# Optimization experiments

Hardware: AMD Instinct MI355X
Metric: run time of the kernel (lower is better)

## Reference

```python
import jax, jax.numpy as jnp
import numpy as np

B, NL, NT = 8, 64, 512   # graphs, ligand atoms/graph, target nodes/graph
CF = 128                 # per-node embedding dim (Linear(256,...) => 2*128)
H = 128                  # hidden_dim
K = 10                   # n_gaussians
E = 1024                 # ligand edges
BN_EPS = 1e-4


def setup_inputs() -> dict:
    key = jax.random.key(0)
    ks = jax.random.split(key, 24)
    inp = {}
    inp["h_l_x"] = jax.random.normal(ks[0], (B * NL, CF), jnp.float32)
    inp["h_t_x"] = jax.random.normal(ks[1], (B * NT, CF), jnp.float32)
    inp["h_l_pos"] = jax.random.normal(ks[2], (B * NL, 3), jnp.float32)
    inp["h_t_pos"] = jax.random.normal(ks[3], (B * NT, 3), jnp.float32)
    inp["edge_index"] = jax.random.randint(ks[4], (2, E), 0, B * NL, jnp.int64)
    s = 0.05
    inp["W1"] = jax.random.normal(ks[5], (2 * CF, H), jnp.float32) * s
    inp["b1"] = jnp.zeros((H,), jnp.float32)
    inp["gamma"] = jnp.ones((H,), jnp.float32)
    inp["beta"] = jnp.zeros((H,), jnp.float32)
    inp["rmean"] = jax.random.normal(ks[6], (H,), jnp.float32) * 0.1
    inp["rvar"] = jax.random.uniform(ks[7], (H,), jnp.float32, 0.5, 1.5)
    inp["Wpi"] = jax.random.normal(ks[8], (H, K), jnp.float32) * s
    inp["bpi"] = jnp.zeros((K,), jnp.float32)
    inp["Wsig"] = jax.random.normal(ks[9], (H, K), jnp.float32) * s
    inp["bsig"] = jnp.zeros((K,), jnp.float32)
    inp["Wmu"] = jax.random.normal(ks[10], (H, K), jnp.float32) * s
    inp["bmu"] = jnp.zeros((K,), jnp.float32)
    inp["Wat"] = jax.random.normal(ks[11], (CF, 28), jnp.float32) * s
    inp["bat"] = jnp.zeros((28,), jnp.float32)
    inp["Wbd"] = jax.random.normal(ks[12], (2 * CF, 6), jnp.float32) * s
    inp["bbd"] = jnp.zeros((6,), jnp.float32)
    return inp


def reference(h_l_x, h_t_x, h_l_pos, h_t_pos, edge_index,
              W1, b1, gamma, beta, rmean, rvar,
              Wpi, bpi, Wsig, bsig, Wmu, bmu, Wat, bat, Wbd, bbd):
    # dense batched node features (equal counts per graph => reshape)
    hl = h_l_x.reshape(B, NL, CF)
    ht = h_t_x.reshape(B, NT, CF)

    # cat([hl_repeat, ht_repeat]) @ W1 == hl@W1[:CF] + ht@W1[CF:] (broadcast add)
    zl = jnp.einsum('blc,ch->blh', hl, W1[:CF])          # [B,NL,H]
    zt = jnp.einsum('btc,ch->bth', ht, W1[CF:])          # [B,NT,H]
    z = zl[:, :, None, :] + zt[:, None, :, :] + b1       # [B,NL,NT,H]
    z = z.reshape(B * NL * NT, H)

    # BatchNorm1d (eval: running stats), ELU; Dropout is identity in eval
    z = (z - rmean) * (gamma / jnp.sqrt(rvar + BN_EPS)) + beta
    C = jax.nn.elu(z)

    pi = jax.nn.softmax(C @ Wpi + bpi, axis=-1)
    sigma = jax.nn.elu(C @ Wsig + bsig) + 1.1
    mu = jax.nn.elu(C @ Wmu + bmu) + 1.0

    # pairwise euclidean distances, detached in original
    pl = h_l_pos.reshape(B, NL, 3)
    pt = h_t_pos.reshape(B, NT, 3)
    d2 = (-2.0 * jnp.einsum('bld,btd->blt', pl, pt)
          + jnp.sum(pt ** 2, -1)[:, None, :]
          + jnp.sum(pl ** 2, -1)[:, :, None])
    dist = jnp.sqrt(d2).reshape(B * NL * NT)
    dist = jax.lax.stop_gradient(dist)[:, None]          # [P,1]

    atom_types = h_l_x @ Wat + bat                       # [B*NL,28]
    eb = jnp.concatenate([h_l_x[edge_index[0]], h_l_x[edge_index[1]]], axis=1)
    bond_types = eb @ Wbd + bbd                          # [E,6]

    C_batch = jnp.repeat(jnp.arange(B, dtype=jnp.int32), NL * NT)
    return (pi, sigma, mu, dist, atom_types, bond_types, C_batch)
```

## Files before the change

kernel.cpp:

```cpp
#include <hip/hip_runtime.h>
#include <hip/hip_bf16.h>
#include <cstdint>
#include <cstddef>

#define NB_B 8
#define NL   64
#define NT   512
#define CF   128
#define HD   128
#define NK   10
#define NE   1024

static constexpr size_t P_TOT    = (size_t)NB_B * NL * NT;
static constexpr size_t PI_OFF   = 0;
static constexpr size_t SIG_OFF  = P_TOT * 10;
static constexpr size_t MU_OFF   = SIG_OFF + P_TOT * 10;
static constexpr size_t DIST_OFF = MU_OFF + P_TOT * 10;
static constexpr size_t AT_OFF   = DIST_OFF + P_TOT;
static constexpr size_t BD_OFF   = AT_OFF + 512 * 28;
static constexpr size_t CB_OFF   = BD_OFF + NE * 6;

typedef __attribute__((ext_vector_type(8))) short short8;
typedef __attribute__((ext_vector_type(4))) float floatx4;
typedef __attribute__((ext_vector_type(2))) float floatx2;

union U8 { short8 s8; unsigned int u[4]; };

__device__ __forceinline__ float bf2f(unsigned short u) {
    return __uint_as_float(((unsigned int)u) << 16);
}
__device__ __forceinline__ unsigned short f2bf(float f) {
    unsigned int x = __float_as_uint(f);
    x = (x + 0x7FFFu + ((x >> 16) & 1u)) >> 16;
    return (unsigned short)x;
}
__device__ __forceinline__ unsigned int pk2bf(float a, float b) {
    __hip_bfloat162 h = __float22bfloat162_rn(make_float2(a, b));
    return *reinterpret_cast<unsigned int*>(&h);
}
__device__ __forceinline__ float elu(float x) {
    return fmaxf(x, 0.f) + (__expf(fminf(x, 0.f)) - 1.f);
}

__global__ __launch_bounds__(256) void k_pre(
    const float* __restrict__ hl,
    const float* __restrict__ ht,
    const int*   __restrict__ eidx,
    const float* __restrict__ W1,
    const float* __restrict__ b1,
    const float* __restrict__ gamma_,
    const float* __restrict__ beta_,
    const float* __restrict__ rmean,
    const float* __restrict__ rvar,
    const float* __restrict__ Wpi,
    const float* __restrict__ Wsig,
    const float* __restrict__ Wmu,
    const float* __restrict__ Wat,
    const float* __restrict__ bat,
    const float* __restrict__ Wbd,
    const float* __restrict__ bbd,
    unsigned short* __restrict__ zl,
    unsigned short* __restrict__ zt,
    unsigned short* __restrict__ wcomb_t,
    float* __restrict__ out_at,
    float* __restrict__ out_bd)
{
    const int blk = blockIdx.x;
    const int tid = threadIdx.x;

    if (blk < 144) {
        const bool is_l = (blk < 16);
        const int rbase = is_l ? blk * 32 : (blk - 16) * 32;
        const float* A  = is_l ? hl : ht;
        const float* Wx = W1 + (is_l ? 0 : (size_t)CF * HD);
        unsigned short* Z = is_l ? zl : zt;

        const int wave = tid >> 6;
        const int lane = tid & 63;
        const int m    = lane & 15;
        const int kq   = (lane >> 4) * 8;
        const int n0   = wave * 32 + m;

        floatx4 acc[2][2];
        #pragma unroll
        for (int i = 0; i < 2; ++i)
            #pragma unroll
            for (int j = 0; j < 2; ++j)
                acc[i][j] = (floatx4){0.f, 0.f, 0.f, 0.f};

        #pragma unroll
        for (int kb = 0; kb < 4; ++kb) {
            const int k0 = kb * 32 + kq;
            short8 a[2];
            #pragma unroll
            for (int mt = 0; mt < 2; ++mt) {
                const float* ap = A + (size_t)(rbase + mt * 16 + m) * CF + k0;
                const float4 f0 = *(const float4*)ap;
                const float4 f1 = *(const float4*)(ap + 4);
                U8 t;
                t.u[0] = pk2bf(f0.x, f0.y);
                t.u[1] = pk2bf(f0.z, f0.w);
                t.u[2] = pk2bf(f1.x, f1.y);
                t.u[3] = pk2bf(f1.z, f1.w);
                a[mt] = t.s8;
            }
            short8 bf[2];
            #pragma unroll
            for (int nt = 0; nt < 2; ++nt) {
                const int n = n0 + nt * 16;
                float w[8];
                #pragma unroll
                for (int j = 0; j < 8; ++j)
                    w[j] = Wx[(size_t)(k0 + j) * HD + n];
                U8 t;
                #pragma unroll
                for (int j = 0; j < 4; ++j) t.u[j] = pk2bf(w[2*j], w[2*j+1]);
                bf[nt] = t.s8;
            }
            #pragma unroll
            for (int mt = 0; mt < 2; ++mt)
                #pragma unroll
                for (int nt = 0; nt < 2; ++nt)
                    acc[mt][nt] = __builtin_amdgcn_mfma_f32_16x16x32_bf16(a[mt], bf[nt], acc[mt][nt], 0, 0, 0);
        }

        #pragma unroll
        for (int nt = 0; nt < 2; ++nt) {
            const int col = n0 + nt * 16;
            const float s   = gamma_[col] * rsqrtf(rvar[col] + 1e-4f);
            const float off = is_l ? 0.f : ((b1[col] - rmean[col]) * s + beta_[col]);
            #pragma unroll
            for (int mt = 0; mt < 2; ++mt)
                #pragma unroll
                for (int r = 0; r < 4; ++r) {
                    const int row = rbase + mt * 16 + (lane >> 4) * 4 + r;
                    Z[(size_t)row * HD + col] = f2bf(acc[mt][nt][r] * s + off);
                }
        }
    } else if (blk == 144) {
        for (int i = tid; i < 32 * HD; i += 256) {
            const int n = i >> 7, k = i & 127;
            float v = 0.f;
            if (n < 10)      v = Wpi [k * NK + n];
            else if (n < 20) v = Wsig[k * NK + (n - 10)];
            else if (n < 30) v = Wmu [k * NK + (n - 20)];
            wcomb_t[i] = f2bf(v);
        }
    } else if (blk < 201) {
        const int oi = (blk - 145) * 256 + tid;
        const int r = oi / 28, n = oi - r * 28;
        float acc = bat[n];
        #pragma unroll 4
        for (int c = 0; c < CF; ++c)
            acc += hl[(size_t)r * CF + c] * Wat[c * 28 + n];
        out_at[oi] = acc;
    } else {
        const int oi = (blk - 201) * 256 + tid;
        const int e = oi / 6, n = oi - e * 6;
        const int s0 = eidx[e], s1 = eidx[NE + e];
        float acc = bbd[n];
        #pragma unroll 4
        for (int c = 0; c < CF; ++c) {
            acc += hl[(size_t)s0 * CF + c] * Wbd[c * 6 + n];
            acc += hl[(size_t)s1 * CF + c] * Wbd[(CF + c) * 6 + n];
        }
        out_bd[oi] = acc;
    }
}

__global__ __launch_bounds__(256) void k_main(
    const unsigned short* __restrict__ zl,
    const unsigned short* __restrict__ zt,
    const unsigned short* __restrict__ wcomb_t,
    const float* __restrict__ bpi,
    const float* __restrict__ bsig,
    const float* __restrict__ bmu,
    const float* __restrict__ hlpos,
    const float* __restrict__ htpos,
    float* __restrict__ out)
{
    __shared__ float Dl[128 * 34];
    __shared__ float biass[32];
    __shared__ float pls[3];

    const int tid  = threadIdx.x;
    const int blk  = blockIdx.x;
    const int b    = blk >> 8;
    const int l    = (blk >> 2) & 63;
    const int ch   = blk & 3;
    const int lane = tid & 63;
    const int wave = tid >> 6;
    const int m    = lane & 15;
    const int quad = lane >> 4;

    if (tid < 32) {
        float v = 0.f;
        if (tid < 10)      v = bpi[tid];
        else if (tid < 20) v = bsig[tid - 10];
        else if (tid < 30) v = bmu[tid - 20];
        biass[tid] = v;
    } else if (tid < 35) {
        pls[tid - 32] = hlpos[(size_t)(b * NL + l) * 3 + (tid - 32)];
    }

    short8 bfrag[2][4];
    #pragma unroll
    for (int nt = 0; nt < 2; ++nt)
        #pragma unroll
        for (int kb = 0; kb < 4; ++kb)
            bfrag[nt][kb] = *(const short8*)(wcomb_t + (size_t)(nt * 16 + m) * HD + kb * 32 + quad * 8);

    const unsigned short* zlr = zl + (size_t)(b * NL + l) * HD;
    const unsigned short* ztb = zt + (size_t)(b * NT + ch * 128) * HD;

    floatx4 acc[2][2];
    #pragma unroll
    for (int i = 0; i < 2; ++i)
        #pragma unroll
        for (int j = 0; j < 2; ++j)
            acc[i][j] = (floatx4){0.f, 0.f, 0.f, 0.f};

    #pragma unroll
    for (int kb = 0; kb < 4; ++kb) {
        const int k0 = kb * 32 + quad * 8;
        const short8 zlv = *(const short8*)(zlr + k0);
        float zf[8];
        #pragma unroll
        for (int j = 0; j < 8; ++j) zf[j] = bf2f((unsigned short)zlv[j]);

        short8 a[2];
        #pragma unroll
        for (int mt = 0; mt < 2; ++mt) {
            const int row = wave * 32 + mt * 16 + m;
            const short8 ztv = *(const short8*)(ztb + (size_t)row * HD + k0);
            float e[8];
            #pragma unroll
            for (int j = 0; j < 8; ++j)
                e[j] = elu(zf[j] + bf2f((unsigned short)ztv[j]));
            U8 t;
            #pragma unroll
            for (int j = 0; j < 4; ++j) t.u[j] = pk2bf(e[2*j], e[2*j+1]);
            a[mt] = t.s8;
        }
        #pragma unroll
        for (int mt = 0; mt < 2; ++mt)
            #pragma unroll
            for (int nt = 0; nt < 2; ++nt)
                acc[mt][nt] = __builtin_amdgcn_mfma_f32_16x16x32_bf16(a[mt], bfrag[nt][kb], acc[mt][nt], 0, 0, 0);
    }

    #pragma unroll
    for (int mt = 0; mt < 2; ++mt)
        #pragma unroll
        for (int nt = 0; nt < 2; ++nt)
            #pragma unroll
            for (int r = 0; r < 4; ++r) {
                const int row = wave * 32 + mt * 16 + quad * 4 + r;
                const int col = nt * 16 + m;
                Dl[row * 34 + col] = acc[mt][nt][r];
            }
    __syncthreads();

    const size_t gp = ((size_t)(b * NL + l)) * NT + ch * 128 + (tid & 127);
    if (tid < 128) {
        const int p = tid;
        float v[10];
        float mx = -1e30f;
        #pragma unroll
        for (int n = 0; n < 10; ++n) {
            v[n] = Dl[p * 34 + n] + biass[n];
            mx = fmaxf(mx, v[n]);
        }
        float s = 0.f;
        #pragma unroll
        for (int n = 0; n < 10; ++n) { v[n] = __expf(v[n] - mx); s += v[n]; }
        const float inv = 1.f / s;
        floatx2* po = (floatx2*)(out + PI_OFF + gp * 10);
        #pragma unroll
        for (int n = 0; n < 5; ++n) po[n] = (floatx2){v[2*n] * inv, v[2*n+1] * inv};
    } else {
        const int p = tid - 128;
        float sg[10], mv[10];
        #pragma unroll
        for (int n = 0; n < 10; ++n) {
            sg[n] = elu(Dl[p * 34 + 10 + n] + biass[10 + n]) + 1.1f;
            mv[n] = elu(Dl[p * 34 + 20 + n] + biass[20 + n]) + 1.0f;
        }
        floatx2* ps = (floatx2*)(out + SIG_OFF + gp * 10);
        floatx2* pm = (floatx2*)(out + MU_OFF  + gp * 10);
        #pragma unroll
        for (int n = 0; n < 5; ++n) {
            ps[n] = (floatx2){sg[2*n], sg[2*n+1]};
            pm[n] = (floatx2){mv[2*n], mv[2*n+1]};
        }
        const int t = ch * 128 + p;
        const size_t pb = (size_t)(b * NT + t) * 3;
        const float dx = pls[0] - htpos[pb + 0];
        const float dy = pls[1] - htpos[pb + 1];
        const float dz = pls[2] - htpos[pb + 2];
        out[DIST_OFF + gp] = sqrtf(dx * dx + dy * dy + dz * dz);
        out[CB_OFF + gp]   = (float)b;
    }
}

extern "C" void kernel_launch(void* const* d_in, const int* in_sizes, int n_in,
                              void* d_out, int out_size, void* d_ws, size_t ws_size,
                              hipStream_t stream)
{
    const float* hl     = (const float*)d_in[0];
    const float* ht     = (const float*)d_in[1];
    const float* hlpos  = (const float*)d_in[2];
    const float* htpos  = (const float*)d_in[3];
    const int*   eidx   = (const int*)d_in[4];
    const float* W1     = (const float*)d_in[5];
    const float* b1     = (const float*)d_in[6];
    const float* gamma_ = (const float*)d_in[7];
    const float* beta_  = (const float*)d_in[8];
    const float* rmean  = (const float*)d_in[9];
    const float* rvar   = (const float*)d_in[10];
    const float* Wpi    = (const float*)d_in[11];
    const float* bpi    = (const float*)d_in[12];
    const float* Wsig   = (const float*)d_in[13];
    const float* bsig   = (const float*)d_in[14];
    const float* Wmu    = (const float*)d_in[15];
    const float* bmu    = (const float*)d_in[16];
    const float* Wat    = (const float*)d_in[17];
    const float* bat    = (const float*)d_in[18];
    const float* Wbd    = (const float*)d_in[19];
    const float* bbd    = (const float*)d_in[20];

    float* out = (float*)d_out;
    unsigned short* ws  = (unsigned short*)d_ws;
    unsigned short* zl      = ws;
    unsigned short* zt      = ws + 512 * 128;
    unsigned short* wcomb_t = ws + 512 * 128 + 4096 * 128;

    k_pre<<<225, 256, 0, stream>>>(hl, ht, eidx, W1, b1, gamma_, beta_, rmean, rvar,
                                   Wpi, Wsig, Wmu, Wat, bat, Wbd, bbd,
                                   zl, zt, wcomb_t, out + AT_OFF, out + BD_OFF);
    k_main<<<2048, 256, 0, stream>>>(zl, zt, wcomb_t, bpi, bsig, bmu, hlpos, htpos, out);
}
```

Measured before the change: 140.4 us.

## Move atom/bond head GEMMs into main kernel using bf16 MFMA

The atom-type and bond-type projections move out of the preprocessing kernel and run as 12 extra blocks at the end of the main kernel's grid. They now use bf16 MFMA tiles instead of scalar fp32 dot-product loops. This shortens the serial pre-kernel, which is on the critical path before k_main, and overlaps the small heads with the main work. The cost is bf16 rounding on these outputs, which may reduce accuracy, plus uncoalesced weight loads.

```diff
diff --git a/kernel.cpp b/kernel.cpp
--- a/kernel.cpp
+++ b/kernel.cpp
@@ -45,7 +45,6 @@
 __global__ __launch_bounds__(256) void k_pre(
     const float* __restrict__ hl,
     const float* __restrict__ ht,
-    const int*   __restrict__ eidx,
     const float* __restrict__ W1,
     const float* __restrict__ b1,
     const float* __restrict__ gamma_,
@@ -55,15 +54,9 @@
     const float* __restrict__ Wpi,
     const float* __restrict__ Wsig,
     const float* __restrict__ Wmu,
-    const float* __restrict__ Wat,
-    const float* __restrict__ bat,
-    const float* __restrict__ Wbd,
-    const float* __restrict__ bbd,
     unsigned short* __restrict__ zl,
     unsigned short* __restrict__ zt,
-    unsigned short* __restrict__ wcomb_t,
-    float* __restrict__ out_at,
-    float* __restrict__ out_bd)
+    unsigned short* __restrict__ wcomb_t)
 {
     const int blk = blockIdx.x;
     const int tid = threadIdx.x;
@@ -137,7 +130,7 @@
                     Z[(size_t)row * HD + col] = f2bf(acc[mt][nt][r] * s + off);
                 }
         }
-    } else if (blk == 144) {
+    } else {
         for (int i = tid; i < 32 * HD; i += 256) {
             const int n = i >> 7, k = i & 127;
             float v = 0.f;
@@ -146,25 +139,6 @@
             else if (n < 30) v = Wmu [k * NK + (n - 20)];
             wcomb_t[i] = f2bf(v);
         }
-    } else if (blk < 201) {
-        const int oi = (blk - 145) * 256 + tid;
-        const int r = oi / 28, n = oi - r * 28;
-        float acc = bat[n];
-        #pragma unroll 4
-        for (int c = 0; c < CF; ++c)
-            acc += hl[(size_t)r * CF + c] * Wat[c * 28 + n];
-        out_at[oi] = acc;
-    } else {
-        const int oi = (blk - 201) * 256 + tid;
-        const int e = oi / 6, n = oi - e * 6;
-        const int s0 = eidx[e], s1 = eidx[NE + e];
-        float acc = bbd[n];
-        #pragma unroll 4
-        for (int c = 0; c < CF; ++c) {
-            acc += hl[(size_t)s0 * CF + c] * Wbd[c * 6 + n];
-            acc += hl[(size_t)s1 * CF + c] * Wbd[(CF + c) * 6 + n];
-        }
-        out_bd[oi] = acc;
     }
 }
 
@@ -177,6 +151,12 @@
     const float* __restrict__ bmu,
     const float* __restrict__ hlpos,
     const float* __restrict__ htpos,
+    const float* __restrict__ hl,
+    const int*   __restrict__ eidx,
+    const float* __restrict__ Wat,
+    const float* __restrict__ bat,
+    const float* __restrict__ Wbd,
+    const float* __restrict__ bbd,
     float* __restrict__ out)
 {
     __shared__ float Dl[128 * 34];
@@ -185,13 +165,122 @@
 
     const int tid  = threadIdx.x;
     const int blk  = blockIdx.x;
-    const int b    = blk >> 8;
-    const int l    = (blk >> 2) & 63;
-    const int ch   = blk & 3;
     const int lane = tid & 63;
     const int wave = tid >> 6;
     const int m    = lane & 15;
     const int quad = lane >> 4;
+
+    if (blk >= 2048) {
+        const int ab = blk - 2048;
+        if (ab < 4) {
+            const int rbase = ab * 128 + wave * 32;
+            floatx4 acc[2][2];
+            #pragma unroll
+            for (int i = 0; i < 2; ++i)
+                #pragma unroll
+                for (int j = 0; j < 2; ++j)
+                    acc[i][j] = (floatx4){0.f, 0.f, 0.f, 0.f};
+            #pragma unroll
+            for (int kb = 0; kb < 4; ++kb) {
+                const int k0 = kb * 32 + quad * 8;
+                short8 a[2];
+                #pragma unroll
+                for (int mt = 0; mt < 2; ++mt) {
+                    const float* ap = hl + (size_t)(rbase + mt * 16 + m) * CF + k0;
+                    const float4 f0 = *(const float4*)ap;
+                    const float4 f1 = *(const float4*)(ap + 4);
+                    U8 t;
+                    t.u[0] = pk2bf(f0.x, f0.y);
+                    t.u[1] = pk2bf(f0.z, f0.w);
+                    t.u[2] = pk2bf(f1.x, f1.y);
+                    t.u[3] = pk2bf(f1.z, f1.w);
+                    a[mt] = t.s8;
+                }
+                short8 bf[2];
+                #pragma unroll
+                for (int nt = 0; nt < 2; ++nt) {
+                    const int n = nt * 16 + m;
+                    const int nc = (n < 28) ? n : 0;
+                    #pragma unroll
+                    for (int j = 0; j < 8; ++j) {
+                        const float w = Wat[(size_t)(k0 + j) * 28 + nc];
+                        bf[nt][j] = (short)f2bf((n < 28) ? w : 0.f);
+                    }
+                }
+                #pragma unroll
+                for (int mt = 0; mt < 2; ++mt)
+                    #pragma unroll
+                    for (int nt = 0; nt < 2; ++nt)
+                        acc[mt][nt] = __builtin_amdgcn_mfma_f32_16x16x32_bf16(a[mt], bf[nt], acc[mt][nt], 0, 0, 0);
+            }
+            #pragma unroll
+            for (int nt = 0; nt < 2; ++nt) {
+                const int col = nt * 16 + m;
+                if (col < 28) {
+                    const float bias = bat[col];
+                    #pragma unroll
+                    for (int mt = 0; mt < 2; ++mt)
+                        #pragma unroll
+                        for (int r = 0; r < 4; ++r) {
+                            const int row = rbase + mt * 16 + quad * 4 + r;
+                            out[AT_OFF + (size_t)row * 28 + col] = acc[mt][nt][r] + bias;
+                        }
+                }
+            }
+        } else {
+            const int rbase = (ab - 4) * 128 + wave * 32;
+            const int e0 = rbase + m, e1 = rbase + 16 + m;
+            const int s00 = eidx[e0], s01 = eidx[NE + e0];
+            const int s10 = eidx[e1], s11 = eidx[NE + e1];
+            floatx4 acc[2];
+            acc[0] = (floatx4){0.f, 0.f, 0.f, 0.f};
+            acc[1] = (floatx4){0.f, 0.f, 0.f, 0.f};
+            const int nc = (m < 6) ? m : 0;
+            #pragma unroll
+            for (int kb = 0; kb < 8; ++kb) {
+                const int k0 = kb * 32 + quad * 8;
+                const bool lo = (k0 < 128);
+                const int off = lo ? k0 : (k0 - 128);
+                short8 a[2];
+                #pragma unroll
+                for (int mt = 0; mt < 2; ++mt) {
+                    const int src = lo ? (mt ? s10 : s00) : (mt ? s11 : s01);
+                    const float* ap = hl + (size_t)src * CF + off;
+                    const float4 f0 = *(const float4*)ap;
+                    const float4 f1 = *(const float4*)(ap + 4);
+                    U8 t;
+                    t.u[0] = pk2bf(f0.x, f0.y);
+                    t.u[1] = pk2bf(f0.z, f0.w);
+                    t.u[2] = pk2bf(f1.x, f1.y);
+                    t.u[3] = pk2bf(f1.z, f1.w);
+                    a[mt] = t.s8;
+                }
+                short8 bf;
+                #pragma unroll
+                for (int j = 0; j < 8; ++j) {
+                    const float w = Wbd[(size_t)(k0 + j) * 6 + nc];
+                    bf[j] = (short)f2bf((m < 6) ? w : 0.f);
+                }
+                acc[0] = __builtin_amdgcn_mfma_f32_16x16x32_bf16(a[0], bf, acc[0], 0, 0, 0);
+                acc[1] = __builtin_amdgcn_mfma_f32_16x16x32_bf16(a[1], bf, acc[1], 0, 0, 0);
+            }
+            if (m < 6) {
+                const float bias = bbd[m];
+                #pragma unroll
+                for (int mt = 0; mt < 2; ++mt)
+                    #pragma unroll
+                    for (int r = 0; r < 4; ++r) {
+                        const int row = rbase + mt * 16 + quad * 4 + r;
+                        out[BD_OFF + (size_t)row * 6 + m] = acc[mt][r] + bias;
+                    }
+            }
+        }
+        return;
+    }
+
+    const int b  = blk >> 8;
+    const int l  = (blk >> 2) & 63;
+    const int ch = blk & 3;
 
     if (tid < 32) {
         float v = 0.f;
@@ -335,8 +424,8 @@
     unsigned short* zt      = ws + 512 * 128;
     unsigned short* wcomb_t = ws + 512 * 128 + 4096 * 128;
 
-    k_pre<<<225, 256, 0, stream>>>(hl, ht, eidx, W1, b1, gamma_, beta_, rmean, rvar,
-                                   Wpi, Wsig, Wmu, Wat, bat, Wbd, bbd,
-                                   zl, zt, wcomb_t, out + AT_OFF, out + BD_OFF);
-    k_main<<<2048, 256, 0, stream>>>(zl, zt, wcomb_t, bpi, bsig, bmu, hlpos, htpos, out);
-}
+    k_pre<<<145, 256, 0, stream>>>(hl, ht, W1, b1, gamma_, beta_, rmean, rvar,
+                                   Wpi, Wsig, Wmu, zl, zt, wcomb_t);
+    k_main<<<2060, 256, 0, stream>>>(zl, zt, wcomb_t, bpi, bsig, bmu, hlpos, htpos,
+                                     hl, eidx, Wat, bat, Wbd, bbd, out);
+}
```

After: 132.3 us. -5.7%, faster.
